# Kernel tuning notes

Hardware: AMD Instinct MI355X
Metric: run time of the kernel (lower is better)

Reference implementation:

```python
import jax, jax.numpy as jnp
import numpy as np

N = 100000   # nodes
E = 1600000  # edges
D = 64       # in/hidden channels


def setup_inputs() -> dict:
    key = jax.random.key(0)
    ks = jax.random.split(key, 8)
    x = jax.random.normal(ks[0], (N, D), dtype=jnp.float32)
    edge_index = jax.random.randint(ks[1], (2, E), 0, N, dtype=jnp.int32)
    s = 1.0 / np.sqrt(D)
    W1 = jax.random.uniform(ks[2], (D, D), jnp.float32, -s, s)
    W2 = jax.random.uniform(ks[3], (D, D), jnp.float32, -s, s)
    W3 = jax.random.uniform(ks[4], (D, D), jnp.float32, -s, s)
    b1 = jnp.zeros((D,), jnp.float32)
    b2 = jnp.zeros((D,), jnp.float32)
    b3 = jnp.zeros((D,), jnp.float32)
    return {"x": x, "edge_index": edge_index,
            "W1": W1, "b1": b1, "W2": W2, "b2": b2, "W3": W3, "b3": b3}


def _gcn_conv(x, src, dst, deg_inv_sqrt, W, b):
    # norm = d^{-1/2}[src] * d^{-1/2}[dst] (symmetric GCN normalization w/ self-loops)
    norm = deg_inv_sqrt[src] * deg_inv_sqrt[dst]        # [E+N]
    h = x @ W                                           # [N, D] dense GEMM
    msg = h[src] * norm[:, None]                        # gather + scale
    out = jax.ops.segment_sum(msg, dst, num_segments=x.shape[0])  # scatter-add
    return out + b


def reference(x, edge_index, W1, b1, W2, b2, W3, b3):
    n = x.shape[0]
    loop = jnp.arange(n, dtype=edge_index.dtype)
    src = jnp.concatenate([edge_index[0], loop])        # add self-loops
    dst = jnp.concatenate([edge_index[1], loop])
    deg = jax.ops.segment_sum(jnp.ones_like(src, x.dtype), dst, num_segments=n)
    deg_inv_sqrt = jnp.where(deg > 0, jax.lax.rsqrt(jnp.maximum(deg, 1.0)), 0.0)

    h = _gcn_conv(x, src, dst, deg_inv_sqrt, W1, b1)
    h = jax.nn.relu(h)                                  # dropout is identity (eval)
    h = _gcn_conv(h, src, dst, deg_inv_sqrt, W2, b2)
    h = jax.nn.relu(h)
    out = _gcn_conv(h, src, dst, deg_inv_sqrt, W3, b3)
    return out
```

## Files before the change

### kernel.cpp

```cpp
#include <hip/hip_runtime.h>
#include <hip/hip_fp16.h>
#include <type_traits>

#define DCH 64
#define NBSHIFT 8
#define BROWS 256
#define MAXNB 512
#define CAPB 5120
#define CAP 8192
#define CHUNK 4096

__global__ void init_cursor(int* __restrict__ cursor, int NB) {
    int i = blockIdx.x * blockDim.x + threadIdx.x;
    if (i < NB) cursor[i] = i * CAPB;
}

__global__ __launch_bounds__(256) void bucket_scatter(const int* __restrict__ src,
        const int* __restrict__ dst, int* __restrict__ cursor,
        unsigned int* __restrict__ tmp, int E, int NB) {
    __shared__ int hist[MAXNB];
    __shared__ int res[MAXNB];
    const int base_e = blockIdx.x * CHUNK;
    const int nloc = min(CHUNK, E - base_e);
    for (int i = threadIdx.x; i < NB; i += blockDim.x) hist[i] = 0;
    __syncthreads();
    for (int i = threadIdx.x; i < nloc; i += blockDim.x)
        atomicAdd(&hist[dst[base_e + i] >> NBSHIFT], 1);
    __syncthreads();
    for (int i = threadIdx.x; i < NB; i += blockDim.x) {
        int c = hist[i];
        res[i] = c ? atomicAdd(&cursor[i], c) : 0;
        hist[i] = 0;
    }
    __syncthreads();
    for (int i = threadIdx.x; i < nloc; i += blockDim.x) {
        int d = dst[base_e + i];
        int b = d >> NBSHIFT;
        int r = atomicAdd(&hist[b], 1);
        unsigned int packed = ((unsigned int)(d & (BROWS - 1)) << 24) |
                              (unsigned int)src[base_e + i];
        tmp[res[b] + r] = packed;
    }
}

__global__ __launch_bounds__(BROWS) void bucket_to_csr(
        const unsigned int* __restrict__ tmp, const int* __restrict__ cursor,
        int* __restrict__ rowbeg, int* __restrict__ rowend,
        int* __restrict__ srcs, float* __restrict__ dinv, int N) {
    __shared__ int hist[BROWS];
    __shared__ int off[BROWS];
    __shared__ int cur[BROWS];
    __shared__ int stage[CAP];
    const int b = blockIdx.x;
    const int base = b * CAPB;
    const int count = cursor[b] - base;
    const int t = threadIdx.x;
    hist[t] = 0;
    __syncthreads();
    for (int i = t; i < count; i += BROWS)
        atomicAdd(&hist[tmp[base + i] >> 24], 1);
    __syncthreads();
    int v = hist[t];
    off[t] = v;
    __syncthreads();
    for (int o = 1; o < BROWS; o <<= 1) {
        int add = (t >= o) ? off[t - o] : 0;
        __syncthreads();
        off[t] += add;
        __syncthreads();
    }
    int excl = off[t] - v;
    cur[t] = excl;
    int node = (b << NBSHIFT) + t;
    if (node < N) {
        rowbeg[node] = base + excl;
        rowend[node] = base + excl + v;
        dinv[node]   = rsqrtf((float)v + 1.0f);
    }
    __syncthreads();
    const bool st = (count <= CAP);
    for (int i = t; i < count; i += BROWS) {
        unsigned int p = tmp[base + i];
        int low = p >> 24;
        int s = (int)(p & 0xFFFFFFu);
        int pos = atomicAdd(&cur[low], 1);
        if (st) stage[pos] = s;
        else    srcs[base + pos] = s;
    }
    __syncthreads();
    if (st)
        for (int i = t; i < count; i += BROWS) srcs[base + i] = stage[i];
}

template<typename InT>
__global__ __launch_bounds__(256, 4) void gemm64(const InT* __restrict__ A,
        const float* __restrict__ W, const float* __restrict__ dinv,
        __half* __restrict__ H, int nrows) {
    __shared__ float Wl[64 * 64];
    __shared__ float Al[64 * 68];
    #pragma unroll
    for (int j = 0; j < 4; ++j) {
        int idx = (int)threadIdx.x + j * 256;
        float4 w = ((const float4*)W)[idx];
        int k = idx >> 4, c = (idx & 15) * 4;
        *(float4*)&Wl[k * 64 + c] = w;
    }
    const int tx = threadIdx.x & 15;
    const int ty = threadIdx.x >> 4;
    const int c0 = tx * 4, r0 = ty * 4;
    const int ntiles = (nrows + 63) >> 6;
    for (int tile = blockIdx.x; tile < ntiles; tile += gridDim.x) {
        const int rowbase = tile << 6;
        const int rmax = min(64, nrows - rowbase);
        __syncthreads();
        #pragma unroll
        for (int j = 0; j < 4; ++j) {
            int idx = (int)threadIdx.x + j * 256;
            int r = idx >> 4, kq = idx & 15;
            float4 a;
            if (r < rmax) {
                if constexpr (std::is_same<InT, float>::value) {
                    a = *(const float4*)(A + (size_t)(rowbase + r) * 64 + kq * 4);
                } else {
                    unsigned long long u = *(const unsigned long long*)
                        ((const __half*)A + (size_t)(rowbase + r) * 64 + kq * 4);
                    union { unsigned long long u; __half2 h[2]; } cv; cv.u = u;
                    float2 f0 = __half22float2(cv.h[0]);
                    float2 f1 = __half22float2(cv.h[1]);
                    a = make_float4(f0.x, f0.y, f1.x, f1.y);
                }
            } else a = make_float4(0.f, 0.f, 0.f, 0.f);
            *(float4*)&Al[r * 68 + kq * 4] = a;
        }
        __syncthreads();
        float acc[4][4] = {};
        #pragma unroll 8
        for (int k = 0; k < 64; ++k) {
            float4 wv = *(const float4*)&Wl[k * 64 + c0];
            float a0 = Al[(r0 + 0) * 68 + k];
            float a1 = Al[(r0 + 1) * 68 + k];
            float a2 = Al[(r0 + 2) * 68 + k];
            float a3 = Al[(r0 + 3) * 68 + k];
            acc[0][0] += a0 * wv.x; acc[0][1] += a0 * wv.y; acc[0][2] += a0 * wv.z; acc[0][3] += a0 * wv.w;
            acc[1][0] += a1 * wv.x; acc[1][1] += a1 * wv.y; acc[1][2] += a1 * wv.z; acc[1][3] += a1 * wv.w;
            acc[2][0] += a2 * wv.x; acc[2][1] += a2 * wv.y; acc[2][2] += a2 * wv.z; acc[2][3] += a2 * wv.w;
            acc[3][0] += a3 * wv.x; acc[3][1] += a3 * wv.y; acc[3][2] += a3 * wv.z; acc[3][3] += a3 * wv.w;
        }
        #pragma unroll
        for (int i = 0; i < 4; ++i) {
            int r = r0 + i;
            if (r < rmax) {
                float s = dinv[rowbase + r];
                __half2* ph = (__half2*)(H + (size_t)(rowbase + r) * 64 + c0);
                ph[0] = __floats2half2_rn(acc[i][0] * s, acc[i][1] * s);
                ph[1] = __floats2half2_rn(acc[i][2] * s, acc[i][3] * s);
            }
        }
    }
}

__device__ __forceinline__ void accumh(__half2 acc[4], float4 v) {
    const __half2* hp = (const __half2*)&v;
    #pragma unroll
    for (int j = 0; j < 4; ++j) acc[j] = __hadd2(acc[j], hp[j]);
}

__device__ __forceinline__ float4 row16(const __half* __restrict__ hs, int s, int q) {
    return *(const float4*)((const char*)hs + ((size_t)s << 7) + (q << 4));
}

template<typename OutT>
__global__ __launch_bounds__(256) void aggregate(
    const __half* __restrict__ hs, const int* __restrict__ rowbeg,
    const int* __restrict__ rowend, const int* __restrict__ srcs,
    const float* __restrict__ dinv, const float* __restrict__ b,
    OutT* __restrict__ out, int n, int do_relu)
{
    int wid  = (blockIdx.x * blockDim.x + threadIdx.x) >> 6;
    int lane = threadIdx.x & 63;
    if (wid >= n) return;
    const int g = lane >> 3;
    const int q = lane & 7;
    int beg = rowbeg[wid], end = rowend[wid];
    __half2 zero = __float2half2_rn(0.f);
    __half2 acch[4]  = {zero, zero, zero, zero};
    __half2 acch2[4] = {zero, zero, zero, zero};
    if (g == 7) accumh(acch, row16(hs, wid, q));
    int e = beg + g;
    for (; e + 8 < end; e += 16) {
        int s0 = srcs[e];
        int s1 = srcs[e + 8];
        float4 v0 = row16(hs, s0, q);
        float4 v1 = row16(hs, s1, q);
        accumh(acch, v0);
        accumh(acch2, v1);
    }
    if (e < end) accumh(acch, row16(hs, srcs[e], q));
    float acc[8];
    #pragma unroll
    for (int j = 0; j < 4; ++j) {
        float2 f0 = __half22float2(acch[j]);
        float2 f1 = __half22float2(acch2[j]);
        acc[2 * j]     = f0.x + f1.x;
        acc[2 * j + 1] = f0.y + f1.y;
    }
    #pragma unroll
    for (int j = 0; j < 8; ++j) {
        float a = acc[j];
        a += __shfl_xor(a, 8);
        a += __shfl_xor(a, 16);
        a += __shfl_xor(a, 32);
        acc[j] = a;
    }
    if (g == 0) {
        float dd = dinv[wid];
        float o[8];
        #pragma unroll
        for (int j = 0; j < 8; ++j) {
            float v = acc[j] * dd + b[q * 8 + j];
            o[j] = do_relu ? fmaxf(v, 0.f) : v;
        }
        if constexpr (std::is_same<OutT, __half>::value) {
            union { uint4 u; __half2 h[4]; } cv;
            cv.h[0] = __floats2half2_rn(o[0], o[1]);
            cv.h[1] = __floats2half2_rn(o[2], o[3]);
            cv.h[2] = __floats2half2_rn(o[4], o[5]);
            cv.h[3] = __floats2half2_rn(o[6], o[7]);
            *(uint4*)((__half*)out + (size_t)wid * DCH + q * 8) = cv.u;
        } else {
            float4* po = (float4*)((float*)out + (size_t)wid * DCH + q * 8);
            po[0] = make_float4(o[0], o[1], o[2], o[3]);
            po[1] = make_float4(o[4], o[5], o[6], o[7]);
        }
    }
}

extern "C" void kernel_launch(void* const* d_in, const int* in_sizes, int n_in,
                              void* d_out, int out_size, void* d_ws, size_t ws_size,
                              hipStream_t stream) {
    const float* x  = (const float*)d_in[0];
    const int*   ei = (const int*)d_in[1];
    const float* W1 = (const float*)d_in[2];
    const float* b1 = (const float*)d_in[3];
    const float* W2 = (const float*)d_in[4];
    const float* b2 = (const float*)d_in[5];
    const float* W3 = (const float*)d_in[6];
    const float* b3 = (const float*)d_in[7];

    const int N = in_sizes[0] / DCH;
    const int E = in_sizes[1] / 2;
    const int* src = ei;
    const int* dst = ei + E;
    const int NB = (N + BROWS - 1) >> NBSHIFT;

    char* ws = (char*)d_ws;
    size_t off = 0;
    auto alloc = [&](size_t bytes) { void* p = ws + off; off = (off + bytes + 255) & ~(size_t)255; return p; };
    int*    cursor = (int*)   alloc((size_t)MAXNB * 4);
    int*    rowbeg = (int*)   alloc((size_t)N * 4);
    int*    rowend = (int*)   alloc((size_t)N * 4);
    int*    srcs   = (int*)   alloc((size_t)NB * CAPB * 4);
    float*  dinv   = (float*) alloc((size_t)N * 4);
    __half* hs     = (__half*)alloc((size_t)N * DCH * 2);
    __half* agg    = (__half*)alloc((size_t)N * DCH * 2);
    unsigned int* tmp = (unsigned int*)hs;
    float* out = (float*)d_out;

    const int T = 256;
    const int gAG  = (N * DCH + T - 1) / T;
    const int gGM  = (N + 63) / 64;
    const int nchk = (E + CHUNK - 1) / CHUNK;

    init_cursor<<<(NB + T - 1) / T, T, 0, stream>>>(cursor, NB);
    bucket_scatter<<<nchk, T, 0, stream>>>(src, dst, cursor, tmp, E, NB);
    bucket_to_csr<<<NB, BROWS, 0, stream>>>(tmp, cursor, rowbeg, rowend, srcs, dinv, N);

    gemm64<float><<<gGM, T, 0, stream>>>(x, W1, dinv, hs, N);
    aggregate<__half><<<gAG, T, 0, stream>>>(hs, rowbeg, rowend, srcs, dinv, b1, agg, N, 1);

    gemm64<__half><<<gGM, T, 0, stream>>>(agg, W2, dinv, hs, N);
    aggregate<__half><<<gAG, T, 0, stream>>>(hs, rowbeg, rowend, srcs, dinv, b2, agg, N, 1);

    gemm64<__half><<<gGM, T, 0, stream>>>(agg, W3, dinv, hs, N);
    aggregate<float><<<gAG, T, 0, stream>>>(hs, rowbeg, rowend, srcs, dinv, b3, out, N, 0);
}
```

Before: 229.0 us.

## Shrink CSR buckets, pack row ranges into int2, memset cursors

Halves the bucket width to 128 rows, which doubles the bucket count and makes each bucket_to_csr block smaller. Row begin and end are packed into one int2 so each aggregate warp needs a single load. The init kernel is replaced by a memset of relative cursors, with the bucket base added during scatter. Smaller buckets raise parallelism in CSR construction, but they mean more global atomics on cursors and a tighter per-bucket capacity margin.

```diff
diff --git a/kernel.cpp b/kernel.cpp
--- a/kernel.cpp
+++ b/kernel.cpp
@@ -3,17 +3,12 @@
 #include <type_traits>
 
 #define DCH 64
-#define NBSHIFT 8
-#define BROWS 256
-#define MAXNB 512
-#define CAPB 5120
-#define CAP 8192
-#define CHUNK 4096
-
-__global__ void init_cursor(int* __restrict__ cursor, int NB) {
-    int i = blockIdx.x * blockDim.x + threadIdx.x;
-    if (i < NB) cursor[i] = i * CAPB;
-}
+#define NBSHIFT 7
+#define BROWS 128
+#define MAXNB 1024
+#define CAPB 2816
+#define CAP 4096
+#define CHUNK 2048
 
 __global__ __launch_bounds__(256) void bucket_scatter(const int* __restrict__ src,
         const int* __restrict__ dst, int* __restrict__ cursor,
@@ -29,7 +24,7 @@
     __syncthreads();
     for (int i = threadIdx.x; i < NB; i += blockDim.x) {
         int c = hist[i];
-        res[i] = c ? atomicAdd(&cursor[i], c) : 0;
+        res[i] = c ? (i * CAPB + atomicAdd(&cursor[i], c)) : 0;
         hist[i] = 0;
     }
     __syncthreads();
@@ -45,15 +40,15 @@
 
 __global__ __launch_bounds__(BROWS) void bucket_to_csr(
         const unsigned int* __restrict__ tmp, const int* __restrict__ cursor,
-        int* __restrict__ rowbeg, int* __restrict__ rowend,
-        int* __restrict__ srcs, float* __restrict__ dinv, int N) {
+        int2* __restrict__ range, int* __restrict__ srcs,
+        float* __restrict__ dinv, int N) {
     __shared__ int hist[BROWS];
     __shared__ int off[BROWS];
     __shared__ int cur[BROWS];
     __shared__ int stage[CAP];
     const int b = blockIdx.x;
     const int base = b * CAPB;
-    const int count = cursor[b] - base;
+    const int count = cursor[b];
     const int t = threadIdx.x;
     hist[t] = 0;
     __syncthreads();
@@ -73,9 +68,8 @@
     cur[t] = excl;
     int node = (b << NBSHIFT) + t;
     if (node < N) {
-        rowbeg[node] = base + excl;
-        rowend[node] = base + excl + v;
-        dinv[node]   = rsqrtf((float)v + 1.0f);
+        range[node] = make_int2(base + excl, base + excl + v);
+        dinv[node]  = rsqrtf((float)v + 1.0f);
     }
     __syncthreads();
     const bool st = (count <= CAP);
@@ -102,8 +96,7 @@
     for (int j = 0; j < 4; ++j) {
         int idx = (int)threadIdx.x + j * 256;
         float4 w = ((const float4*)W)[idx];
-        int k = idx >> 4, c = (idx & 15) * 4;
-        *(float4*)&Wl[k * 64 + c] = w;
+        *(float4*)&Wl[(idx >> 4) * 64 + (idx & 15) * 4] = w;
     }
     const int tx = threadIdx.x & 15;
     const int ty = threadIdx.x >> 4;
@@ -171,17 +164,17 @@
 
 template<typename OutT>
 __global__ __launch_bounds__(256) void aggregate(
-    const __half* __restrict__ hs, const int* __restrict__ rowbeg,
-    const int* __restrict__ rowend, const int* __restrict__ srcs,
-    const float* __restrict__ dinv, const float* __restrict__ b,
-    OutT* __restrict__ out, int n, int do_relu)
+    const __half* __restrict__ hs, const int2* __restrict__ range,
+    const int* __restrict__ srcs, const float* __restrict__ dinv,
+    const float* __restrict__ b, OutT* __restrict__ out, int n, int do_relu)
 {
     int wid  = (blockIdx.x * blockDim.x + threadIdx.x) >> 6;
     int lane = threadIdx.x & 63;
     if (wid >= n) return;
     const int g = lane >> 3;
     const int q = lane & 7;
-    int beg = rowbeg[wid], end = rowend[wid];
+    const int2 be = range[wid];
+    const int beg = be.x, end = be.y;
     __half2 zero = __float2half2_rn(0.f);
     __half2 acch[4]  = {zero, zero, zero, zero};
     __half2 acch2[4] = {zero, zero, zero, zero};
@@ -257,8 +250,7 @@
     size_t off = 0;
     auto alloc = [&](size_t bytes) { void* p = ws + off; off = (off + bytes + 255) & ~(size_t)255; return p; };
     int*    cursor = (int*)   alloc((size_t)MAXNB * 4);
-    int*    rowbeg = (int*)   alloc((size_t)N * 4);
-    int*    rowend = (int*)   alloc((size_t)N * 4);
+    int2*   range  = (int2*)  alloc((size_t)N * 8);
     int*    srcs   = (int*)   alloc((size_t)NB * CAPB * 4);
     float*  dinv   = (float*) alloc((size_t)N * 4);
     __half* hs     = (__half*)alloc((size_t)N * DCH * 2);
@@ -271,16 +263,16 @@
     const int gGM  = (N + 63) / 64;
     const int nchk = (E + CHUNK - 1) / CHUNK;
 
-    init_cursor<<<(NB + T - 1) / T, T, 0, stream>>>(cursor, NB);
+    hipMemsetAsync(cursor, 0, (size_t)NB * 4, stream);
     bucket_scatter<<<nchk, T, 0, stream>>>(src, dst, cursor, tmp, E, NB);
-    bucket_to_csr<<<NB, BROWS, 0, stream>>>(tmp, cursor, rowbeg, rowend, srcs, dinv, N);
+    bucket_to_csr<<<NB, BROWS, 0, stream>>>(tmp, cursor, range, srcs, dinv, N);
 
     gemm64<float><<<gGM, T, 0, stream>>>(x, W1, dinv, hs, N);
-    aggregate<__half><<<gAG, T, 0, stream>>>(hs, rowbeg, rowend, srcs, dinv, b1, agg, N, 1);
+    aggregate<__half><<<gAG, T, 0, stream>>>(hs, range, srcs, dinv, b1, agg, N, 1);
 
     gemm64<__half><<<gGM, T, 0, stream>>>(agg, W2, dinv, hs, N);
-    aggregate<__half><<<gAG, T, 0, stream>>>(hs, rowbeg, rowend, srcs, dinv, b2, agg, N, 1);
+    aggregate<__half><<<gAG, T, 0, stream>>>(hs, range, srcs, dinv, b2, agg, N, 1);
 
     gemm64<__half><<<gGM, T, 0, stream>>>(agg, W3, dinv, hs, N);
-    aggregate<float><<<gAG, T, 0, stream>>>(hs, rowbeg, rowend, srcs, dinv, b3, out, N, 0);
-}
+    aggregate<float><<<gAG, T, 0, stream>>>(hs, range, srcs, dinv, b3, out, N, 0);
+}
```

New measurement: 246.4 us. 7.6% more time.
